# Kernel optimization log

Measured on AMD Instinct MI355X. Metric: run time of the kernel, lower is better.

The kernel has to match this reference:

```python
import jax, jax.numpy as jnp
import numpy as np

HIDDEN = 2048
NUM_HEADS = 16
HEAD_DIM = HIDDEN // NUM_HEADS
SCALE = 1.0 / np.sqrt(HEAD_DIM).astype(np.float32)
BATCH, SEQ = 2, 2048


def setup_inputs() -> dict:
    key = jax.random.key(0)
    ks = jax.random.split(key, 9)
    std = 0.02
    inp = {
        'hidden_states': jax.random.normal(ks[0], (BATCH, SEQ, HIDDEN), jnp.float32),
        'attention_mask': jnp.zeros((BATCH, 1, 1, SEQ), jnp.float32),
        'Wq': jax.random.normal(ks[1], (HIDDEN, HIDDEN), jnp.float32) * std,
        'bq': jnp.zeros((HIDDEN,), jnp.float32),
        'Wk': jax.random.normal(ks[2], (HIDDEN, HIDDEN), jnp.float32) * std,
        'bk': jnp.zeros((HIDDEN,), jnp.float32),
        'Wv': jax.random.normal(ks[3], (HIDDEN, HIDDEN), jnp.float32) * std,
        'bv': jnp.zeros((HIDDEN,), jnp.float32),
        'Wo': jax.random.normal(ks[4], (HIDDEN, HIDDEN), jnp.float32) * std,
        'bo': jnp.zeros((HIDDEN,), jnp.float32),
    }
    return inp


def _split_heads(x):
    b, s, _ = x.shape
    return x.reshape(b, s, NUM_HEADS, HEAD_DIM).transpose(0, 2, 1, 3)  # [b,h,s,d]


def reference(hidden_states, attention_mask, Wq, bq, Wk, bk, Wv, bv, Wo, bo):
    # Linear layers (torch convention: y = x @ W.T + b)
    q = _split_heads(hidden_states @ Wq.T + bq)
    k = _split_heads(hidden_states @ Wk.T + bk)
    v = _split_heads(hidden_states @ Wv.T + bv)
    scores = jnp.einsum('bhqd,bhkd->bhqk', q, k) * SCALE
    scores = scores + attention_mask
    weights = jax.nn.softmax(scores, axis=-1)  # dropout is identity in eval
    ctx = jnp.einsum('bhqk,bhkd->bhqd', weights, v)
    b, h, s, d = ctx.shape
    ctx = ctx.transpose(0, 2, 1, 3).reshape(b, s, HIDDEN)
    return ctx @ Wo.T + bo
```

## Files before the change

### kernel.cpp

```cpp
#include <hip/hip_runtime.h>

typedef __bf16 bf16_t;
typedef bf16_t bf16x8 __attribute__((ext_vector_type(8)));
typedef float f32x4 __attribute__((ext_vector_type(4)));

#define HIDDEN 2048
#define SEQ 2048
#define BATCH 2
#define NHEADS 16
#define HDIM 128
#define MTOT (BATCH*SEQ)
#define SCALE 0.088388347648318447f
#define C1EXP2 0.12753102158508967f
#define LOG2E  1.4426950408889634f

__device__ __forceinline__ float dev_exp2(float x) { return __builtin_amdgcn_exp2f(x); }

typedef __attribute__((address_space(1))) const void gvoid_t;
typedef __attribute__((address_space(3))) void svoid_t;
__device__ __forceinline__ void async_copy16(const bf16_t* g, bf16_t* l) {
  __builtin_amdgcn_global_load_lds((gvoid_t*)g, (svoid_t*)l, 16, 0, 0);
}

__global__ void cvt_all(const float* __restrict__ x,  const float* __restrict__ wq,
                        const float* __restrict__ wk, const float* __restrict__ wv,
                        const float* __restrict__ wo,
                        bf16_t* __restrict__ xb, bf16_t* __restrict__ wqkb,
                        bf16_t* __restrict__ wvb, bf16_t* __restrict__ wob) {
  const size_t HH = (size_t)HIDDEN * HIDDEN;
  const float* src; bf16_t* dst;
  switch (blockIdx.y) {
    case 0:  src = x;        dst = xb;        break;
    case 1:  src = x + HH;   dst = xb + HH;   break;
    case 2:  src = wq;       dst = wqkb;      break;
    case 3:  src = wk;       dst = wqkb + HH; break;
    case 4:  src = wv;       dst = wvb;       break;
    default: src = wo;       dst = wob;       break;
  }
  int i = blockIdx.x * 256 + threadIdx.x;
  float4 v = reinterpret_cast<const float4*>(src)[i];
  union { bf16_t h[4]; uint2 u; } t;
  t.h[0] = (bf16_t)v.x; t.h[1] = (bf16_t)v.y; t.h[2] = (bf16_t)v.z; t.h[3] = (bf16_t)v.w;
  reinterpret_cast<uint2*>(dst)[i] = t.u;
}

__global__ void pack_bias2(const float* __restrict__ a, const float* __restrict__ b2,
                           float* __restrict__ out) {
  int i = blockIdx.x * 256 + threadIdx.x;
  out[i] = (i < HIDDEN) ? a[i] : b2[i - HIDDEN];
}

#define RD_A(dst, buf, mh) do {                                                \
  _Pragma("unroll") for (int mi_ = 0; mi_ < 4; ++mi_)                          \
    _Pragma("unroll") for (int kk_ = 0; kk_ < 2; ++kk_)                        \
      dst[mi_][kk_] = *(const bf16x8*)&As[buf][mh][(wr * 64 + mi_ * 16 + lr) * 64 \
                         + (((kk_ * 4 + quad) ^ (lr & 7)) * 8)];               \
} while (0)
#define RD_B(dst, buf, nh) do {                                                \
  _Pragma("unroll") for (int ni_ = 0; ni_ < 2; ++ni_)                          \
    _Pragma("unroll") for (int kk_ = 0; kk_ < 2; ++kk_)                        \
      dst[ni_][kk_] = *(const bf16x8*)&Bs[buf][nh][(wc * 32 + ni_ * 16 + lr) * 64 \
                         + (((kk_ * 4 + quad) ^ (lr & 7)) * 8)];               \
} while (0)
#define MMQ(mh, nh, afr, bfr) do {                                             \
  __builtin_amdgcn_s_setprio(1);                                               \
  _Pragma("unroll") for (int mi_ = 0; mi_ < 4; ++mi_)                          \
    _Pragma("unroll") for (int ni_ = 0; ni_ < 2; ++ni_) {                      \
      acc[(mh)*4 + mi_][(nh)*2 + ni_] = __builtin_amdgcn_mfma_f32_16x16x32_bf16( \
          afr[mi_][0], bfr[ni_][0], acc[(mh)*4 + mi_][(nh)*2 + ni_], 0, 0, 0); \
      acc[(mh)*4 + mi_][(nh)*2 + ni_] = __builtin_amdgcn_mfma_f32_16x16x32_bf16( \
          afr[mi_][1], bfr[ni_][1], acc[(mh)*4 + mi_][(nh)*2 + ni_], 0, 0, 0); \
    }                                                                          \
  __builtin_amdgcn_s_setprio(0);                                               \
} while (0)
#define STG(ptr, t64, ldsbase) do {                                            \
  async_copy16((ptr) + (t64), (ldsbase));                                      \
  async_copy16((ptr) + (size_t)8 * K + (t64), (ldsbase) + 8 * 64);             \
} while (0)
#define PHASE_SYNC do { __builtin_amdgcn_s_barrier();                          \
  asm volatile("s_waitcnt lgkmcnt(0)" ::: "memory");                           \
  __builtin_amdgcn_sched_barrier(0); } while (0)

template<bool OUT_BF16, bool ROW_BIAS>
__global__ __launch_bounds__(512)
void gemm8p(const bf16_t* __restrict__ A, const bf16_t* __restrict__ Bt,
            const float* __restrict__ bias, void* __restrict__ Yv,
            int K, int ldY, int nbt) {
  __shared__ __align__(16) bf16_t As[2][2][128 * 64];
  __shared__ __align__(16) bf16_t Bs[2][2][128 * 64];
  const int tid  = threadIdx.x;
  const int lane = tid & 63;
  const int wv   = tid >> 6;
  const int wr   = wv >> 2, wc = wv & 3;
  const int lr   = lane & 15, quad = lane >> 4;

  const int wg  = blockIdx.x;
  const int cpx = gridDim.x >> 3;
  const int swz = (wg & 7) * cpx + (wg >> 3);
  const int m0  = (swz / nbt) * 256;
  const int n0  = (swz % nbt) * 256;

  f32x4 acc[8][4] = {};

  const int sub = lane >> 3, chv = (lane & 7) ^ sub;
  const int rih = wv * 16 + sub;
  const bf16_t* pA0 = A  + (size_t)(m0 +       rih) * K + chv * 8;
  const bf16_t* pA1 = A  + (size_t)(m0 + 128 + rih) * K + chv * 8;
  const bf16_t* pB0 = Bt + (size_t)(n0 +       rih) * K + chv * 8;
  const bf16_t* pB1 = Bt + (size_t)(n0 + 128 + rih) * K + chv * 8;
  const int lwo = wv * 16 * 64;
  const int nt  = K >> 6;

  STG(pB0, (size_t)0,  &Bs[0][0][lwo]);
  STG(pA0, (size_t)0,  &As[0][0][lwo]);
  STG(pA1, (size_t)0,  &As[0][1][lwo]);
  STG(pB1, (size_t)0,  &Bs[0][1][lwo]);
  STG(pB0, (size_t)64, &Bs[1][0][lwo]);
  STG(pA0, (size_t)64, &As[1][0][lwo]);
  asm volatile("s_waitcnt vmcnt(2)" ::: "memory");
  __builtin_amdgcn_s_barrier();

  bf16x8 af0[4][2], af1[4][2], bf0[2][2], bf1[2][2];

  for (int t = 0; t < nt; ++t) {
    const int p = t & 1;
    const size_t tk = (size_t)t * 64;

    RD_A(af0, p, 0); RD_B(bf0, p, 0);
    if (t + 1 < nt) STG(pA1, tk + 64, &As[p ^ 1][1][lwo]);
    PHASE_SYNC; MMQ(0, 0, af0, bf0); __builtin_amdgcn_s_barrier();

    RD_A(af1, p, 1);
    if (t + 1 < nt) STG(pB1, tk + 64, &Bs[p ^ 1][1][lwo]);
    PHASE_SYNC; MMQ(1, 0, af1, bf0); __builtin_amdgcn_s_barrier();

    RD_B(bf1, p, 1);
    if (t + 2 < nt) STG(pB0, tk + 128, &Bs[p][0][lwo]);
    PHASE_SYNC; MMQ(0, 1, af0, bf1); __builtin_amdgcn_s_barrier();

    if (t + 2 < nt) {
      STG(pA0, tk + 128, &As[p][0][lwo]);
      asm volatile("s_waitcnt vmcnt(4)" ::: "memory");
    } else {
      asm volatile("s_waitcnt vmcnt(0)" ::: "memory");
    }
    PHASE_SYNC; MMQ(1, 1, af1, bf1); __builtin_amdgcn_s_barrier();
  }

  float bc[4];
  if (!ROW_BIAS) {
#pragma unroll
    for (int fn = 0; fn < 4; ++fn)
      bc[fn] = bias[n0 + (fn >> 1) * 128 + wc * 32 + (fn & 1) * 16 + lr];
  }
#pragma unroll
  for (int fm = 0; fm < 8; ++fm) {
    const int rowb = m0 + (fm >> 2) * 128 + wr * 64 + (fm & 3) * 16 + quad * 4;
#pragma unroll
    for (int r = 0; r < 4; ++r) {
      const int row = rowb + r;
      const float brow = ROW_BIAS ? bias[row] : 0.0f;
      const size_t base = (size_t)row * ldY;
#pragma unroll
      for (int fn = 0; fn < 4; ++fn) {
        const int col = n0 + (fn >> 1) * 128 + wc * 32 + (fn & 1) * 16 + lr;
        float y = acc[fm][fn][r] + (ROW_BIAS ? brow : bc[fn]);
        if (OUT_BF16) ((bf16_t*)Yv)[base + col] = (bf16_t)y;
        else          ((float*)Yv)[base + col]  = y;
      }
    }
  }
}

#define BQ 128
#define BKV 64
#define LDQK 4096

__global__ __launch_bounds__(256, 2)
void attn_kernel(const bf16_t* __restrict__ QK, const bf16_t* __restrict__ Vt,
                 const float* __restrict__ mask, bf16_t* __restrict__ O) {
  __shared__ __align__(16) bf16_t Ks[2][BKV * 128];
  __shared__ __align__(16) bf16_t Vs[HDIM * BKV];
  __shared__ __align__(16) bf16_t Ps[BQ * BKV];
  __shared__ __align__(16) float  Msk[SEQ];

  const int tid  = threadIdx.x;
  const int lane = tid & 63;
  const int wv   = tid >> 6;
  const int lr   = lane & 15, quad = lane >> 4;
  const int q0   = blockIdx.x * BQ;
  const int bh   = blockIdx.y;
  const int b    = bh >> 4, h = bh & 15;

  const bf16_t* Qg = QK + (size_t)(b * SEQ + q0) * LDQK + h * HDIM;
  const bf16_t* Kg = QK + (size_t)(b * SEQ) * LDQK + HIDDEN + h * HDIM;
  const bf16_t* Vg = Vt + (size_t)(h * HDIM) * MTOT + b * SEQ;
  const float*  mb = mask + b * SEQ;

  bf16x8 qf[2][4];
#pragma unroll
  for (int mi = 0; mi < 2; ++mi)
#pragma unroll
    for (int dk = 0; dk < 4; ++dk)
      qf[mi][dk] = *(const bf16x8*)(Qg + (size_t)(wv * 32 + mi * 16 + lr) * LDQK + dk * 32 + quad * 8);

  for (int i = tid; i < SEQ / 4; i += 256) {
    float4 mv = reinterpret_cast<const float4*>(mb)[i];
    Msk[i * 4 + 0] = mv.x * LOG2E;
    Msk[i * 4 + 1] = mv.y * LOG2E;
    Msk[i * 4 + 2] = mv.z * LOG2E;
    Msk[i * 4 + 3] = mv.w * LOG2E;
  }

  const int kcs = lane & 15;
  const int vcs = lane & 7;
  const bf16_t* kgp[4]; const bf16_t* vgp[4];
  int lKo[4], lVo[4];
#pragma unroll
  for (int i = 0; i < 4; ++i) {
    int kr = wv * 16 + i * 4 + (lane >> 4);
    kgp[i] = Kg + (size_t)kr * LDQK + ((kcs ^ (kr & 15)) * 8);
    lKo[i] = (wv * 16 + i * 4) * 128;
    int vr = wv * 32 + i * 8 + (lane >> 3);
    vgp[i] = Vg + (size_t)vr * MTOT + ((vcs ^ (vr & 7)) * 8);
    lVo[i] = (wv * 32 + i * 8) * 64;
  }

  asm volatile("s_waitcnt vmcnt(0)" ::: "memory");
#pragma unroll
  for (int i = 0; i < 4; ++i) async_copy16(kgp[i], &Ks[0][lKo[i]]);
  asm volatile("s_waitcnt lgkmcnt(0)" ::: "memory");
  __builtin_amdgcn_s_barrier();

  float l_st[2][4] = {};
  f32x4 oacc[2][8] = {};

  for (int kt = 0; kt < SEQ; kt += BKV) {
    const int cur = (kt >> 6) & 1;
    const bf16_t* Kc = &Ks[cur][0];

    asm volatile("s_waitcnt lgkmcnt(0)" ::: "memory");
    __builtin_amdgcn_s_barrier();
#pragma unroll
    for (int i = 0; i < 4; ++i) async_copy16(vgp[i] + kt, &Vs[lVo[i]]);
    if (kt + BKV < SEQ) {
#pragma unroll
      for (int i = 0; i < 4; ++i)
        async_copy16(kgp[i] + (size_t)(kt + BKV) * LDQK, &Ks[cur ^ 1][lKo[i]]);
      asm volatile("s_waitcnt vmcnt(8)" ::: "memory");
    } else {
      asm volatile("s_waitcnt vmcnt(4)" ::: "memory");
    }
    __builtin_amdgcn_s_barrier();
    __builtin_amdgcn_sched_barrier(0);

    float mk[4];
#pragma unroll
    for (int ni = 0; ni < 4; ++ni) mk[ni] = Msk[kt + ni * 16 + lr];

    f32x4 sacc[2][4] = {};
#pragma unroll
    for (int dk = 0; dk < 4; ++dk) {
      bf16x8 kf[4];
#pragma unroll
      for (int ni = 0; ni < 4; ++ni)
        kf[ni] = *(const bf16x8*)&Kc[(ni * 16 + lr) * 128 + (((dk * 4 + quad) ^ lr) * 8)];
#pragma unroll
      for (int mi = 0; mi < 2; ++mi)
#pragma unroll
        for (int ni = 0; ni < 4; ++ni)
          sacc[mi][ni] = __builtin_amdgcn_mfma_f32_16x16x32_bf16(qf[mi][dk], kf[ni], sacc[mi][ni], 0, 0, 0);
    }

#pragma unroll
    for (int mi = 0; mi < 2; ++mi) {
#pragma unroll
      for (int r = 0; r < 4; ++r) {
        float p0 = dev_exp2(fmaf(sacc[mi][0][r], C1EXP2, mk[0]));
        float p1 = dev_exp2(fmaf(sacc[mi][1][r], C1EXP2, mk[1]));
        float p2 = dev_exp2(fmaf(sacc[mi][2][r], C1EXP2, mk[2]));
        float p3 = dev_exp2(fmaf(sacc[mi][3][r], C1EXP2, mk[3]));
        int pr = wv * 32 + mi * 16 + quad * 4 + r;
        int key = pr & 7;
        Ps[pr * BKV + (((0 + (lr >> 3)) ^ key) * 8) + (lr & 7)] = (bf16_t)p0;
        Ps[pr * BKV + (((2 + (lr >> 3)) ^ key) * 8) + (lr & 7)] = (bf16_t)p1;
        Ps[pr * BKV + (((4 + (lr >> 3)) ^ key) * 8) + (lr & 7)] = (bf16_t)p2;
        Ps[pr * BKV + (((6 + (lr >> 3)) ^ key) * 8) + (lr & 7)] = (bf16_t)p3;
        l_st[mi][r] += (p0 + p1) + (p2 + p3);
      }
    }

    if (kt + BKV < SEQ) {
      asm volatile("s_waitcnt vmcnt(4)" ::: "memory");
    } else {
      asm volatile("s_waitcnt vmcnt(0)" ::: "memory");
    }
    __builtin_amdgcn_s_barrier();
    __builtin_amdgcn_sched_barrier(0);

#pragma unroll
    for (int ki = 0; ki < 2; ++ki) {
      bf16x8 pf[2];
#pragma unroll
      for (int mi = 0; mi < 2; ++mi)
        pf[mi] = *(const bf16x8*)&Ps[(wv * 32 + mi * 16 + lr) * BKV + (((ki * 4 + quad) ^ (lr & 7)) * 8)];
#pragma unroll
      for (int di = 0; di < 8; ++di) {
        bf16x8 vf = *(const bf16x8*)&Vs[(di * 16 + lr) * BKV + (((ki * 4 + quad) ^ (lr & 7)) * 8)];
#pragma unroll
        for (int mi = 0; mi < 2; ++mi)
          oacc[mi][di] = __builtin_amdgcn_mfma_f32_16x16x32_bf16(pf[mi], vf, oacc[mi][di], 0, 0, 0);
      }
    }
  }

  bf16_t* Ob = O + (size_t)(b * SEQ + q0) * HIDDEN + h * HDIM;
#pragma unroll
  for (int mi = 0; mi < 2; ++mi) {
#pragma unroll
    for (int r = 0; r < 4; ++r) {
      float s = l_st[mi][r];
      s += __shfl_xor(s, 1);
      s += __shfl_xor(s, 2);
      s += __shfl_xor(s, 4);
      s += __shfl_xor(s, 8);
      float inv = 1.0f / s;
      size_t rowoff = (size_t)(wv * 32 + mi * 16 + quad * 4 + r) * HIDDEN;
#pragma unroll
      for (int di = 0; di < 8; ++di)
        Ob[rowoff + di * 16 + lr] = (bf16_t)(oacc[mi][di][r] * inv);
    }
  }
}

extern "C" void kernel_launch(void* const* d_in, const int* in_sizes, int n_in,
                              void* d_out, int out_size, void* d_ws, size_t ws_size,
                              hipStream_t stream) {
  const float* x   = (const float*)d_in[0];
  const float* msk = (const float*)d_in[1];
  const float* Wq  = (const float*)d_in[2];
  const float* bq  = (const float*)d_in[3];
  const float* Wk  = (const float*)d_in[4];
  const float* bk  = (const float*)d_in[5];
  const float* Wv  = (const float*)d_in[6];
  const float* bv  = (const float*)d_in[7];
  const float* Wo  = (const float*)d_in[8];
  const float* bo  = (const float*)d_in[9];
  float* out = (float*)d_out;

  bf16_t* Xb   = (bf16_t*)d_ws;
  bf16_t* Wqkb = Xb   + (size_t)MTOT * HIDDEN;
  bf16_t* Wvb  = Wqkb + (size_t)2 * HIDDEN * HIDDEN;
  bf16_t* Wob  = Wvb  + (size_t)HIDDEN * HIDDEN;
  bf16_t* QKo  = Wob  + (size_t)HIDDEN * HIDDEN;
  bf16_t* Vto  = QKo  + (size_t)MTOT * 2 * HIDDEN;
  float*  bqk  = (float*)(Vto + (size_t)HIDDEN * MTOT);
  bf16_t* Cb   = Xb;

  cvt_all<<<dim3(HIDDEN * HIDDEN / 4 / 256, 6), 256, 0, stream>>>(
      x, Wq, Wk, Wv, Wo, Xb, Wqkb, Wvb, Wob);
  pack_bias2<<<2 * HIDDEN / 256, 256, 0, stream>>>(bq, bk, bqk);

  gemm8p<true, false><<<256, 512, 0, stream>>>(Xb, Wqkb, bqk, QKo, HIDDEN, 4096, 16);
  gemm8p<true, true><<<128, 512, 0, stream>>>(Wvb, Xb, bv, Vto, HIDDEN, 4096, 16);
  attn_kernel<<<dim3(SEQ / BQ, BATCH * NHEADS), 256, 0, stream>>>(QKo, Vto, msk, Cb);
  gemm8p<false, false><<<128, 512, 0, stream>>>(Cb, Wob, bo, out, HIDDEN, 2048, 8);
}
```

Baseline: 421.5 us.

## Add 256x128 triple-buffered GEMM for V and output projections

Adds a gemm_tall kernel with 256x128 tiles and a three-stage LDS ring buffer, and uses it for the V projection and the output projection. Those two GEMMs now launch 256 workgroups instead of 128, so more of the GPU's compute units get work. The QK GEMM is specialised to compile-time K and ldY, and its phase order is changed so it keeps one A fragment set live instead of two, which cuts register pressure. The cost is lower per-tile data reuse in the smaller-tile GEMMs and more LDS per block for the extra buffer stage.

```diff
diff --git a/kernel.cpp b/kernel.cpp
--- a/kernel.cpp
+++ b/kernel.cpp
@@ -50,6 +50,7 @@
   out[i] = (i < HIDDEN) ? a[i] : b2[i - HIDDEN];
 }
 
+#define QKK 2048
 #define RD_A(dst, buf, mh) do {                                                \
   _Pragma("unroll") for (int mi_ = 0; mi_ < 4; ++mi_)                          \
     _Pragma("unroll") for (int kk_ = 0; kk_ < 2; ++kk_)                        \
@@ -75,17 +76,15 @@
 } while (0)
 #define STG(ptr, t64, ldsbase) do {                                            \
   async_copy16((ptr) + (t64), (ldsbase));                                      \
-  async_copy16((ptr) + (size_t)8 * K + (t64), (ldsbase) + 8 * 64);             \
+  async_copy16((ptr) + (size_t)8 * QKK + (t64), (ldsbase) + 8 * 64);           \
 } while (0)
 #define PHASE_SYNC do { __builtin_amdgcn_s_barrier();                          \
   asm volatile("s_waitcnt lgkmcnt(0)" ::: "memory");                           \
   __builtin_amdgcn_sched_barrier(0); } while (0)
 
-template<bool OUT_BF16, bool ROW_BIAS>
 __global__ __launch_bounds__(512)
 void gemm8p(const bf16_t* __restrict__ A, const bf16_t* __restrict__ Bt,
-            const float* __restrict__ bias, void* __restrict__ Yv,
-            int K, int ldY, int nbt) {
+            const float* __restrict__ bias, bf16_t* __restrict__ Y) {
   __shared__ __align__(16) bf16_t As[2][2][128 * 64];
   __shared__ __align__(16) bf16_t Bs[2][2][128 * 64];
   const int tid  = threadIdx.x;
@@ -95,21 +94,20 @@
   const int lr   = lane & 15, quad = lane >> 4;
 
   const int wg  = blockIdx.x;
-  const int cpx = gridDim.x >> 3;
-  const int swz = (wg & 7) * cpx + (wg >> 3);
-  const int m0  = (swz / nbt) * 256;
-  const int n0  = (swz % nbt) * 256;
+  const int swz = (wg & 7) * 32 + (wg >> 3);
+  const int m0  = (swz >> 4) * 256;
+  const int n0  = (swz & 15) * 256;
 
   f32x4 acc[8][4] = {};
 
   const int sub = lane >> 3, chv = (lane & 7) ^ sub;
   const int rih = wv * 16 + sub;
-  const bf16_t* pA0 = A  + (size_t)(m0 +       rih) * K + chv * 8;
-  const bf16_t* pA1 = A  + (size_t)(m0 + 128 + rih) * K + chv * 8;
-  const bf16_t* pB0 = Bt + (size_t)(n0 +       rih) * K + chv * 8;
-  const bf16_t* pB1 = Bt + (size_t)(n0 + 128 + rih) * K + chv * 8;
+  const bf16_t* pA0 = A  + (size_t)(m0 +       rih) * QKK + chv * 8;
+  const bf16_t* pA1 = A  + (size_t)(m0 + 128 + rih) * QKK + chv * 8;
+  const bf16_t* pB0 = Bt + (size_t)(n0 +       rih) * QKK + chv * 8;
+  const bf16_t* pB1 = Bt + (size_t)(n0 + 128 + rih) * QKK + chv * 8;
   const int lwo = wv * 16 * 64;
-  const int nt  = K >> 6;
+  const int nt  = QKK >> 6;
 
   STG(pB0, (size_t)0,  &Bs[0][0][lwo]);
   STG(pA0, (size_t)0,  &As[0][0][lwo]);
@@ -120,23 +118,23 @@
   asm volatile("s_waitcnt vmcnt(2)" ::: "memory");
   __builtin_amdgcn_s_barrier();
 
-  bf16x8 af0[4][2], af1[4][2], bf0[2][2], bf1[2][2];
+  bf16x8 afr[4][2], bf0[2][2], bf1[2][2];
 
   for (int t = 0; t < nt; ++t) {
     const int p = t & 1;
     const size_t tk = (size_t)t * 64;
 
-    RD_A(af0, p, 0); RD_B(bf0, p, 0);
+    RD_A(afr, p, 0); RD_B(bf0, p, 0);
     if (t + 1 < nt) STG(pA1, tk + 64, &As[p ^ 1][1][lwo]);
-    PHASE_SYNC; MMQ(0, 0, af0, bf0); __builtin_amdgcn_s_barrier();
-
-    RD_A(af1, p, 1);
+    PHASE_SYNC; MMQ(0, 0, afr, bf0); __builtin_amdgcn_s_barrier();
+
+    RD_B(bf1, p, 1);
     if (t + 1 < nt) STG(pB1, tk + 64, &Bs[p ^ 1][1][lwo]);
-    PHASE_SYNC; MMQ(1, 0, af1, bf0); __builtin_amdgcn_s_barrier();
-
-    RD_B(bf1, p, 1);
+    PHASE_SYNC; MMQ(0, 1, afr, bf1); __builtin_amdgcn_s_barrier();
+
+    RD_A(afr, p, 1);
     if (t + 2 < nt) STG(pB0, tk + 128, &Bs[p][0][lwo]);
-    PHASE_SYNC; MMQ(0, 1, af0, bf1); __builtin_amdgcn_s_barrier();
+    PHASE_SYNC; MMQ(1, 1, afr, bf1); __builtin_amdgcn_s_barrier();
 
     if (t + 2 < nt) {
       STG(pA0, tk + 128, &As[p][0][lwo]);
@@ -144,18 +142,114 @@
     } else {
       asm volatile("s_waitcnt vmcnt(0)" ::: "memory");
     }
-    PHASE_SYNC; MMQ(1, 1, af1, bf1); __builtin_amdgcn_s_barrier();
+    PHASE_SYNC; MMQ(1, 0, afr, bf0); __builtin_amdgcn_s_barrier();
+  }
+
+  float bc[4];
+#pragma unroll
+  for (int fn = 0; fn < 4; ++fn)
+    bc[fn] = bias[n0 + (fn >> 1) * 128 + wc * 32 + (fn & 1) * 16 + lr];
+#pragma unroll
+  for (int fm = 0; fm < 8; ++fm) {
+    const int rowb = m0 + (fm >> 2) * 128 + wr * 64 + (fm & 3) * 16 + quad * 4;
+#pragma unroll
+    for (int r = 0; r < 4; ++r) {
+      const size_t base = (size_t)(rowb + r) * 4096;
+#pragma unroll
+      for (int fn = 0; fn < 4; ++fn) {
+        const int col = n0 + (fn >> 1) * 128 + wc * 32 + (fn & 1) * 16 + lr;
+        Y[base + col] = (bf16_t)(acc[fm][fn][r] + bc[fn]);
+      }
+    }
+  }
+}
+
+#define TSTG(ptr, t64, ldsbase) do {                                           \
+  async_copy16((ptr) + (t64), (ldsbase));                                      \
+  async_copy16((ptr) + (size_t)8 * K + (t64), (ldsbase) + 8 * 64);             \
+} while (0)
+#define TRD(kk) do {                                                           \
+  _Pragma("unroll") for (int fi_ = 0; fi_ < 4; ++fi_)                          \
+    af[fi_] = *(const bf16x8*)&As[buf][(wr * 64 + fi_ * 16 + lr) * 64          \
+                  + ((((kk) * 4 + quad) ^ (lr & 7)) * 8)];                     \
+  _Pragma("unroll") for (int fi_ = 0; fi_ < 4; ++fi_)                          \
+    bf[fi_] = *(const bf16x8*)&Bs[buf][(wc * 64 + fi_ * 16 + lr) * 64          \
+                  + ((((kk) * 4 + quad) ^ (lr & 7)) * 8)];                     \
+} while (0)
+#define TMM() do {                                                             \
+  __builtin_amdgcn_s_setprio(1);                                               \
+  _Pragma("unroll") for (int fm_ = 0; fm_ < 4; ++fm_)                          \
+    _Pragma("unroll") for (int fn_ = 0; fn_ < 4; ++fn_)                        \
+      acc[fm_][fn_] = __builtin_amdgcn_mfma_f32_16x16x32_bf16(                 \
+          af[fm_], bf[fn_], acc[fm_][fn_], 0, 0, 0);                           \
+  __builtin_amdgcn_s_setprio(0);                                               \
+} while (0)
+
+template<bool OUT_BF16, bool ROW_BIAS>
+__global__ __launch_bounds__(512)
+void gemm_tall(const bf16_t* __restrict__ A, const bf16_t* __restrict__ Bt,
+               const float* __restrict__ bias, void* __restrict__ Yv,
+               int K, int ldY, int nbt) {
+  __shared__ __align__(16) bf16_t As[3][256 * 64];
+  __shared__ __align__(16) bf16_t Bs[3][128 * 64];
+  const int tid  = threadIdx.x;
+  const int lane = tid & 63;
+  const int wv   = tid >> 6;
+  const int wr   = wv >> 1, wc = wv & 1;
+  const int lr   = lane & 15, quad = lane >> 4;
+
+  const int wg  = blockIdx.x;
+  const int swz = (wg & 7) * 32 + (wg >> 3);
+  const int m0  = (swz / nbt) * 256;
+  const int n0  = (swz % nbt) * 128;
+
+  f32x4 acc[4][4] = {};
+
+  const int sub = lane >> 3, chv = (lane & 7) ^ sub;
+  const int rih = wv * 16 + sub;
+  const bf16_t* pA = A  + (size_t)(m0 + rih) * K + chv * 8;
+  const bf16_t* pB = Bt + (size_t)(n0 + rih) * K + chv * 8;
+  const size_t a1off = (size_t)128 * K;
+  const int lwo = wv * 16 * 64;
+  const int nt  = K >> 6;
+
+  TSTG(pA,         (size_t)0,  &As[0][lwo]);
+  TSTG(pA + a1off, (size_t)0,  &As[0][128 * 64 + lwo]);
+  TSTG(pB,         (size_t)0,  &Bs[0][lwo]);
+  TSTG(pA,         (size_t)64, &As[1][lwo]);
+  TSTG(pA + a1off, (size_t)64, &As[1][128 * 64 + lwo]);
+  TSTG(pB,         (size_t)64, &Bs[1][lwo]);
+  asm volatile("s_waitcnt vmcnt(6)" ::: "memory");
+  __builtin_amdgcn_s_barrier();
+
+  bf16x8 af[4], bf[4];
+  for (int t = 0; t < nt; ++t) {
+    const int buf = t % 3;
+
+    TRD(0);
+    if (t + 2 < nt) {
+      const int b2 = (buf < 1) ? buf + 2 : buf - 1;
+      const size_t tk2 = (size_t)(t + 2) * 64;
+      TSTG(pA,         tk2, &As[b2][lwo]);
+      TSTG(pA + a1off, tk2, &As[b2][128 * 64 + lwo]);
+      TSTG(pB,         tk2, &Bs[b2][lwo]);
+    }
+    PHASE_SYNC; TMM(); __builtin_amdgcn_s_barrier();
+
+    TRD(1);
+    if (t + 2 < nt) { asm volatile("s_waitcnt vmcnt(6)" ::: "memory"); }
+    else            { asm volatile("s_waitcnt vmcnt(0)" ::: "memory"); }
+    PHASE_SYNC; TMM(); __builtin_amdgcn_s_barrier();
   }
 
   float bc[4];
   if (!ROW_BIAS) {
 #pragma unroll
-    for (int fn = 0; fn < 4; ++fn)
-      bc[fn] = bias[n0 + (fn >> 1) * 128 + wc * 32 + (fn & 1) * 16 + lr];
-  }
-#pragma unroll
-  for (int fm = 0; fm < 8; ++fm) {
-    const int rowb = m0 + (fm >> 2) * 128 + wr * 64 + (fm & 3) * 16 + quad * 4;
+    for (int fn = 0; fn < 4; ++fn) bc[fn] = bias[n0 + wc * 64 + fn * 16 + lr];
+  }
+#pragma unroll
+  for (int fm = 0; fm < 4; ++fm) {
+    const int rowb = m0 + wr * 64 + fm * 16 + quad * 4;
 #pragma unroll
     for (int r = 0; r < 4; ++r) {
       const int row = rowb + r;
@@ -163,7 +257,7 @@
       const size_t base = (size_t)row * ldY;
 #pragma unroll
       for (int fn = 0; fn < 4; ++fn) {
-        const int col = n0 + (fn >> 1) * 128 + wc * 32 + (fn & 1) * 16 + lr;
+        const int col = n0 + wc * 64 + fn * 16 + lr;
         float y = acc[fm][fn][r] + (ROW_BIAS ? brow : bc[fn]);
         if (OUT_BF16) ((bf16_t*)Yv)[base + col] = (bf16_t)y;
         else          ((float*)Yv)[base + col]  = y;
@@ -361,8 +455,8 @@
       x, Wq, Wk, Wv, Wo, Xb, Wqkb, Wvb, Wob);
   pack_bias2<<<2 * HIDDEN / 256, 256, 0, stream>>>(bq, bk, bqk);
 
-  gemm8p<true, false><<<256, 512, 0, stream>>>(Xb, Wqkb, bqk, QKo, HIDDEN, 4096, 16);
-  gemm8p<true, true><<<128, 512, 0, stream>>>(Wvb, Xb, bv, Vto, HIDDEN, 4096, 16);
+  gemm8p<<<256, 512, 0, stream>>>(Xb, Wqkb, bqk, QKo);
+  gemm_tall<true, true><<<256, 512, 0, stream>>>(Wvb, Xb, bv, Vto, HIDDEN, 4096, 32);
   attn_kernel<<<dim3(SEQ / BQ, BATCH * NHEADS), 256, 0, stream>>>(QKo, Vto, msk, Cb);
-  gemm8p<false, false><<<128, 512, 0, stream>>>(Cb, Wob, bo, out, HIDDEN, 2048, 8);
-}
+  gemm_tall<false, false><<<256, 512, 0, stream>>>(Cb, Wob, bo, out, HIDDEN, 2048, 16);
+}
```

New measurement: 396.8 us. 5.9% less time.
